# Optimization experiments

Hardware: AMD Instinct MI355X
Metric: run time of the kernel (lower is better)

The kernel has to match this reference:

```python
import jax, jax.numpy as jnp
import numpy as np

B, C, D, H, W = 1, 128, 8, 32, 32
NH, HD = 8, 16            # num_heads, head_dim = C // NH
PD, PH, PW = 2, 4, 4      # local patch dims
RD, RH, RW = 2, 2, 2      # global K/V reduction ratios
MLPH = 4 * C              # mlp_ratio = 4
EPS = 1e-5
SCALE = HD ** -0.5


def setup_inputs() -> dict:
    key = jax.random.key(0)
    ks = iter(jax.random.split(key, 16))
    def w(shape, scale=0.02):
        return jax.random.normal(next(ks), shape, jnp.float32) * scale
    inp = {"x": jax.random.normal(next(ks), (B, C, D, H, W), jnp.float32)}
    for p in ("l", "g"):  # local branch / global branch transformer blocks
        inp[f"{p}_n1_g"] = jnp.ones((C,), jnp.float32)
        inp[f"{p}_n1_b"] = jnp.zeros((C,), jnp.float32)
        inp[f"{p}_qkv_w"] = w((3 * C, C))            # Linear(dim, 3*dim, bias=False)
        inp[f"{p}_proj_w"] = w((C, C))
        inp[f"{p}_proj_b"] = jnp.zeros((C,), jnp.float32)
        inp[f"{p}_n2_g"] = jnp.ones((C,), jnp.float32)
        inp[f"{p}_n2_b"] = jnp.zeros((C,), jnp.float32)
        inp[f"{p}_fc1_w"] = w((MLPH, C))
        inp[f"{p}_fc1_b"] = jnp.zeros((MLPH,), jnp.float32)
        inp[f"{p}_fc2_w"] = w((C, MLPH))
        inp[f"{p}_fc2_b"] = jnp.zeros((C,), jnp.float32)
    inp["g_ke_w"] = w((C, C, RD, RH, RW))  # Conv3d(dim, dim, k=stride=(2,2,2), bias=False)
    inp["g_ve_w"] = w((C, C, RD, RH, RW))
    inp["g_nk_g"] = jnp.ones((HD,), jnp.float32)
    inp["g_nk_b"] = jnp.zeros((HD,), jnp.float32)
    inp["g_nv_g"] = jnp.ones((HD,), jnp.float32)
    inp["g_nv_b"] = jnp.zeros((HD,), jnp.float32)
    return inp


def _ln(t, g, b):
    m = t.mean(-1, keepdims=True)
    v = jnp.square(t - m).mean(-1, keepdims=True)
    return (t - m) * jax.lax.rsqrt(v + EPS) * g + b


def _mlp(t, w1, b1, w2, b2):
    return jax.nn.gelu(t @ w1.T + b1, approximate=False) @ w2.T + b2


def _forward(x, l_n1_g, l_n1_b, l_qkv_w, l_proj_w, l_proj_b, l_n2_g, l_n2_b,
             l_fc1_w, l_fc1_b, l_fc2_w, l_fc2_b,
             g_n1_g, g_n1_b, g_qkv_w, g_ke_w, g_ve_w, g_nk_g, g_nk_b,
             g_nv_g, g_nv_b, g_proj_w, g_proj_b, g_n2_g, g_n2_b,
             g_fc1_w, g_fc1_b, g_fc2_w, g_fc2_b):
    nd, nh, nw = D // PD, H // PH, W // PW
    R, Npl = nd * nh * nw, PD * PH * PW
    N = D * H * W

    # ---------------- Local branch ----------------
    # (B,C,D,H,W) -> (B, R, Npl, C) patch tokens
    loc = x.reshape(B, C, nd, PD, nh, PH, nw, PW)
    loc = loc.transpose(0, 2, 4, 6, 3, 5, 7, 1).reshape(B, R, Npl, C)
    y = _ln(loc, l_n1_g, l_n1_b)
    qkv = (y @ l_qkv_w.T).reshape(B, R, Npl, 3, NH, HD).transpose(3, 0, 1, 4, 2, 5)
    q, k, v = qkv[0], qkv[1], qkv[2]  # (B,R,NH,Npl,HD)
    attn = jax.nn.softmax(jnp.einsum('brhnd,brhmd->brhnm', q, k) * SCALE, axis=-1)
    o = jnp.einsum('brhnm,brhmd->brhnd', attn, v)
    # faithful to torch: (attn@v).transpose(-1,-2).reshape(B,R,Npl,C)
    o = jnp.swapaxes(o, -1, -2).reshape(B, R, Npl, C)
    loc = loc + (o @ l_proj_w.T + l_proj_b)
    loc = loc + _mlp(_ln(loc, l_n2_g, l_n2_b), l_fc1_w, l_fc1_b, l_fc2_w, l_fc2_b)
    # back to (B,C,D,H,W)
    loc_y = loc.reshape(B, nd, nh, nw, PD, PH, PW, C)
    loc_y = loc_y.transpose(0, 7, 1, 4, 2, 5, 3, 6).reshape(B, C, D, H, W)

    # ---------------- Global branch ----------------
    g = x.reshape(B, C, N).transpose(0, 2, 1)  # (B,N,C)
    y = _ln(g, g_n1_g, g_n1_b)
    qkv = y @ g_qkv_w.T  # (B,N,3C)
    q, k, v = jnp.split(qkv, 3, axis=-1)
    qh = q.reshape(B, N, NH, HD).transpose(0, 2, 1, 3)  # (B,NH,N,HD)
    dn = ('NCDHW', 'OIDHW', 'NCDHW')
    def _reduce(t, wc):
        tm = t.transpose(0, 2, 1).reshape(B, C, D, H, W)
        tr = jax.lax.conv_general_dilated(tm, wc, (RD, RH, RW), 'VALID',
                                          dimension_numbers=dn)
        nr = tr.shape[2] * tr.shape[3] * tr.shape[4]
        return tr.reshape(B, C, nr).transpose(0, 2, 1).reshape(B, nr, NH, HD).transpose(0, 2, 1, 3)
    kr = _ln(_reduce(k, g_ke_w), g_nk_g, g_nk_b)  # (B,NH,Nr,HD)
    vr = _ln(_reduce(v, g_ve_w), g_nv_g, g_nv_b)
    attn = jax.nn.softmax(jnp.einsum('bhnd,bhmd->bhnm', qh, kr) * SCALE, axis=-1)
    o = jnp.einsum('bhnm,bhmd->bhnd', attn, vr)
    o = o.transpose(0, 2, 1, 3).reshape(B, N, C)
    g = g + (o @ g_proj_w.T + g_proj_b)
    g = g + _mlp(_ln(g, g_n2_g, g_n2_b), g_fc1_w, g_fc1_b, g_fc2_w, g_fc2_b)
    glo_y = g.transpose(0, 2, 1).reshape(B, C, D, H, W)

    # ---------------- Gate ----------------
    return x * jax.nn.sigmoid(loc_y + glo_y)


def reference(x, l_n1_g, l_n1_b, l_qkv_w, l_proj_w, l_proj_b, l_n2_g, l_n2_b,
              l_fc1_w, l_fc1_b, l_fc2_w, l_fc2_b,
              g_n1_g, g_n1_b, g_qkv_w, g_ke_w, g_ve_w, g_nk_g, g_nk_b,
              g_nv_g, g_nv_b, g_proj_w, g_proj_b, g_n2_g, g_n2_b,
              g_fc1_w, g_fc1_b, g_fc2_w, g_fc2_b):
    return _forward(x, l_n1_g, l_n1_b, l_qkv_w, l_proj_w, l_proj_b, l_n2_g, l_n2_b,
                    l_fc1_w, l_fc1_b, l_fc2_w, l_fc2_b,
                    g_n1_g, g_n1_b, g_qkv_w, g_ke_w, g_ve_w, g_nk_g, g_nk_b,
                    g_nv_g, g_nv_b, g_proj_w, g_proj_b, g_n2_g, g_n2_b,
                    g_fc1_w, g_fc1_b, g_fc2_w, g_fc2_b)
```

## Files before the change

kernel.cpp:

```cpp
#include <hip/hip_runtime.h>
#include <math.h>

#define N_TOK 8192
#define C_DIM 128
#define NHD   8
#define HDIM  16
#define NR    1024
#define EPSV  1e-5f
#define QK_SCALE 0.25f

typedef __attribute__((ext_vector_type(8))) short short8;
typedef __attribute__((ext_vector_type(4))) float f32x4;

__device__ __forceinline__ float gelu_f(float v) {
    return 0.5f * v * (1.0f + erff(v * 0.70710678118654752f));
}
__device__ __forceinline__ float uaf(unsigned int u) {
    union { unsigned int u; float f; } x; x.u = u; return x.f;
}
__device__ __forceinline__ short f2b(float v) {
    union { float f; unsigned int u; } x; x.f = v;
    unsigned int r = x.u + 0x7fffu + ((x.u >> 16) & 1u);
    return (short)(r >> 16);
}
__device__ __forceinline__ void ld16bf(const short* p, float* d) {
    uint4 a = *(const uint4*)p;
    uint4 b = *(const uint4*)(p + 8);
    d[0]  = uaf(a.x << 16); d[1]  = uaf(a.x & 0xffff0000u);
    d[2]  = uaf(a.y << 16); d[3]  = uaf(a.y & 0xffff0000u);
    d[4]  = uaf(a.z << 16); d[5]  = uaf(a.z & 0xffff0000u);
    d[6]  = uaf(a.w << 16); d[7]  = uaf(a.w & 0xffff0000u);
    d[8]  = uaf(b.x << 16); d[9]  = uaf(b.x & 0xffff0000u);
    d[10] = uaf(b.y << 16); d[11] = uaf(b.y & 0xffff0000u);
    d[12] = uaf(b.z << 16); d[13] = uaf(b.z & 0xffff0000u);
    d[14] = uaf(b.w << 16); d[15] = uaf(b.w & 0xffff0000u);
}

struct CvtDesc { const float* src; short* dst; int n; int pad; };
struct CvtArgs { CvtDesc d[10]; };
__global__ __launch_bounds__(256) void cvtw_k(CvtArgs a) {
    CvtDesc dd = a.d[blockIdx.y];
    for (int i = blockIdx.x * 256 + threadIdx.x; i < dd.n; i += gridDim.x * 256)
        dd.dst[i] = f2b(dd.src[i]);
}

__global__ __launch_bounds__(256) void transpose_k(const float* __restrict__ x,
                                                   float* __restrict__ xt) {
    __shared__ float tile[32][33];
    int n0 = blockIdx.x * 32, c0 = blockIdx.y * 32;
    int tx = threadIdx.x, ty = threadIdx.y;
#pragma unroll
    for (int k = 0; k < 4; ++k)
        tile[ty + k * 8][tx] = x[(size_t)(c0 + ty + k * 8) * N_TOK + n0 + tx];
    __syncthreads();
#pragma unroll
    for (int k = 0; k < 4; ++k)
        xt[(size_t)(n0 + ty + k * 8) * C_DIM + c0 + tx] = tile[tx][ty + k * 8];
}

__global__ __launch_bounds__(256) void ln_token_k(const float* __restrict__ in,
                                                  const float* __restrict__ g1, const float* __restrict__ b1,
                                                  short* __restrict__ o1,
                                                  const float* __restrict__ g2, const float* __restrict__ b2,
                                                  short* __restrict__ o2) {
    int lane = threadIdx.x & 63;
    int n = blockIdx.x * 4 + (threadIdx.x >> 6);
    float v0 = in[(size_t)n * C_DIM + lane];
    float v1 = in[(size_t)n * C_DIM + 64 + lane];
    float s = v0 + v1, sq = v0 * v0 + v1 * v1;
#pragma unroll
    for (int off = 32; off >= 1; off >>= 1) {
        s += __shfl_xor(s, off);
        sq += __shfl_xor(sq, off);
    }
    float m = s * (1.0f / 128.0f);
    float var = sq * (1.0f / 128.0f) - m * m;
    float rs = rsqrtf(var + EPSV);
    float h0 = (v0 - m) * rs, h1 = (v1 - m) * rs;
    o1[(size_t)n * C_DIM + lane]      = f2b(h0 * g1[lane] + b1[lane]);
    o1[(size_t)n * C_DIM + 64 + lane] = f2b(h1 * g1[lane + 64] + b1[lane + 64]);
    o2[(size_t)n * C_DIM + lane]      = f2b(h0 * g2[lane] + b2[lane]);
    o2[(size_t)n * C_DIM + 64 + lane] = f2b(h1 * g2[lane + 64] + b2[lane + 64]);
}

__global__ __launch_bounds__(256) void ln2_pair_k(const float* __restrict__ in0,
                                                  const float* __restrict__ g0, const float* __restrict__ b0,
                                                  short* __restrict__ o0,
                                                  const float* __restrict__ in1,
                                                  const float* __restrict__ g1, const float* __restrict__ b1,
                                                  short* __restrict__ o1) {
    int blk = blockIdx.x;
    bool sel = blk >= 2048;
    blk &= 2047;
    const float* in = sel ? in1 : in0;
    const float* g  = sel ? g1 : g0;
    const float* b  = sel ? b1 : b0;
    short* o        = sel ? o1 : o0;
    int lane = threadIdx.x & 63;
    int n = blk * 4 + (threadIdx.x >> 6);
    float v0 = in[(size_t)n * C_DIM + lane];
    float v1 = in[(size_t)n * C_DIM + 64 + lane];
    float s = v0 + v1, sq = v0 * v0 + v1 * v1;
#pragma unroll
    for (int off = 32; off >= 1; off >>= 1) {
        s += __shfl_xor(s, off);
        sq += __shfl_xor(sq, off);
    }
    float m = s * (1.0f / 128.0f);
    float var = sq * (1.0f / 128.0f) - m * m;
    float rs = rsqrtf(var + EPSV);
    o[(size_t)n * C_DIM + lane]      = f2b((v0 - m) * rs * g[lane] + b[lane]);
    o[(size_t)n * C_DIM + 64 + lane] = f2b((v1 - m) * rs * g[lane + 64] + b[lane + 64]);
}

struct MArgs {
    const short* A[2]; const short* W[2];
    const float* bias[2]; const float* res[2];
    void* out[2];
};
template <int EPI>
__global__ __launch_bounds__(256) void mgemm_k(MArgs ga, int M, int N, int K, int kslice) {
    int zi    = (EPI == 3) ? (blockIdx.z >> 2) : blockIdx.z;
    int slice = (EPI == 3) ? (blockIdx.z & 3) : 0;
    const short* A = ga.A[zi];
    const short* W = ga.W[zi];
    __shared__ short As[128 * 64];
    __shared__ short Bs[128 * 64];
    int t = threadIdx.x;
    int w = t >> 6, l = t & 63;
    int m0 = blockIdx.x * 128, n0 = blockIdx.y * 128;
    int wm = (w >> 1) * 64, wn = (w & 1) * 64;
    int kbeg = (EPI == 3) ? slice * kslice : 0;
    int kend = kbeg + ((EPI == 3) ? kslice : K);

    f32x4 acc[4][4];
#pragma unroll
    for (int a = 0; a < 4; ++a)
#pragma unroll
        for (int b = 0; b < 4; ++b) acc[a][b] = f32x4{0.f, 0.f, 0.f, 0.f};

    for (int k0 = kbeg; k0 < kend; k0 += 64) {
        __syncthreads();
#pragma unroll
        for (int c = 0; c < 4; ++c) {
            int chunk = c * 256 + t;
            int row = chunk >> 3;
            int slot = chunk & 7;
            int ss = slot ^ (row & 7);
            uint4 av = *(const uint4*)(A + (size_t)(m0 + row) * K + k0 + slot * 8);
            *(uint4*)(As + row * 64 + ss * 8) = av;
            uint4 wv = *(const uint4*)(W + (size_t)(n0 + row) * K + k0 + slot * 8);
            *(uint4*)(Bs + row * 64 + ss * 8) = wv;
        }
        __syncthreads();
#pragma unroll
        for (int kk = 0; kk < 2; ++kk) {
            short8 af[4], bf[4];
            int sl = kk * 4 + (l >> 4);
#pragma unroll
            for (int mf = 0; mf < 4; ++mf) {
                int row = wm + mf * 16 + (l & 15);
                af[mf] = *(const short8*)(As + row * 64 + (sl ^ (row & 7)) * 8);
            }
#pragma unroll
            for (int nf = 0; nf < 4; ++nf) {
                int row = wn + nf * 16 + (l & 15);
                bf[nf] = *(const short8*)(Bs + row * 64 + (sl ^ (row & 7)) * 8);
            }
#pragma unroll
            for (int mf = 0; mf < 4; ++mf)
#pragma unroll
                for (int nf = 0; nf < 4; ++nf)
                    acc[mf][nf] = __builtin_amdgcn_mfma_f32_16x16x32_bf16(
                        af[mf], bf[nf], acc[mf][nf], 0, 0, 0);
        }
    }

#pragma unroll
    for (int mf = 0; mf < 4; ++mf) {
#pragma unroll
        for (int nf = 0; nf < 4; ++nf) {
            int col = n0 + wn + nf * 16 + (l & 15);
#pragma unroll
            for (int j = 0; j < 4; ++j) {
                int row = m0 + wm + mf * 16 + (l >> 4) * 4 + j;
                float v = acc[mf][nf][j];
                if (EPI == 0) {
                    ((short*)ga.out[zi])[(size_t)row * N + col] = f2b(v);
                } else if (EPI == 1) {
                    v += ga.bias[zi][col] + ga.res[zi][(size_t)row * N + col];
                    ((float*)ga.out[zi])[(size_t)row * N + col] = v;
                } else if (EPI == 2) {
                    v = gelu_f(v + ga.bias[zi][col]);
                    ((short*)ga.out[zi])[(size_t)row * N + col] = f2b(v);
                } else {
                    ((float*)ga.out[zi])[(size_t)slice * M * N + (size_t)row * N + col] = v;
                }
            }
        }
    }
}

__global__ __launch_bounds__(256) void local_attn_k(const short* __restrict__ qkv,
                                                    short* __restrict__ ob) {
    __shared__ float ks[NHD][32][HDIM];
    __shared__ float vs[NHD][32][HDIM];
    int m = threadIdx.x, h = threadIdx.y, r = blockIdx.x;
    int zd = r >> 6, zh = (r >> 3) & 7, zw = r & 7;
    int pd = m >> 4, ph = (m >> 2) & 3, pw = m & 3;
    int n = (zd * 2 + pd) * 1024 + (zh * 4 + ph) * 32 + (zw * 4 + pw);
    const short* base = qkv + (size_t)n * 384 + h * HDIM;
    float q[16], kt[16], vt[16];
    ld16bf(base, q);
    ld16bf(base + 128, kt);
    ld16bf(base + 256, vt);
#pragma unroll
    for (int d = 0; d < 16; ++d) { ks[h][m][d] = kt[d]; vs[h][m][d] = vt[d]; }
    __syncthreads();
    float s[32];
#pragma unroll
    for (int j = 0; j < 32; ++j) {
        float d = 0.f;
#pragma unroll
        for (int dd = 0; dd < 16; ++dd) d += q[dd] * ks[h][j][dd];
        s[j] = __expf(d * QK_SCALE);
    }
    float sum = 0.f;
#pragma unroll
    for (int j = 0; j < 32; ++j) sum += s[j];
    float inv = 1.0f / sum;
    float oo[16] = {};
#pragma unroll
    for (int j = 0; j < 32; ++j) {
        float p = s[j] * inv;
#pragma unroll
        for (int dd = 0; dd < 16; ++dd) oo[dd] += p * vs[h][j][dd];
    }
#pragma unroll
    for (int dd = 0; dd < 16; ++dd) {
        int n2 = h * 4 + (dd >> 2);
        int c2 = (dd & 3) * 32 + m;
        int pd2 = n2 >> 4, ph2 = (n2 >> 2) & 3, pw2 = n2 & 3;
        int nn = (zd * 2 + pd2) * 1024 + (zh * 4 + ph2) * 32 + (zw * 4 + pw2);
        ob[(size_t)nn * C_DIM + c2] = f2b(oo[dd]);
    }
}

__global__ __launch_bounds__(256) void gather_k(const short* __restrict__ qkv,
                                                short* __restrict__ kg, short* __restrict__ vg) {
    int idx = blockIdx.x * 256 + threadIdx.x;
    int nr = idx >> 10, qq = idx & 1023;
    int ci = qq >> 3, off = qq & 7;
    int od = off >> 2, oh = (off >> 1) & 1, ow = off & 1;
    int d2 = nr >> 8, h2 = (nr >> 4) & 15, w2 = nr & 15;
    int n = (2 * d2 + od) * 1024 + (2 * h2 + oh) * 32 + (2 * w2 + ow);
    kg[idx] = qkv[(size_t)n * 384 + 128 + ci];
    vg[idx] = qkv[(size_t)n * 384 + 256 + ci];
}

__global__ __launch_bounds__(256) void ln_head_sum_k(const float* __restrict__ kpart,
                                                     const float* __restrict__ vpart,
                                                     const float* __restrict__ gk, const float* __restrict__ bk,
                                                     const float* __restrict__ gv, const float* __restrict__ bv,
                                                     short* __restrict__ kout, short* __restrict__ vout) {
    int idx = blockIdx.x * 256 + threadIdx.x;
    bool sel = idx >= 8192;
    int id2 = idx & 8191;
    const float* part = sel ? vpart : kpart;
    const float* g    = sel ? gv : gk;
    const float* b    = sel ? bv : bk;
    int nr = id2 >> 3, h = id2 & 7;
    size_t base = (size_t)nr * C_DIM + h * HDIM;
    float v[16] = {};
#pragma unroll
    for (int p = 0; p < 4; ++p) {
        const float* pp = part + (size_t)p * (NR * C_DIM) + base;
#pragma unroll
        for (int d4 = 0; d4 < 4; ++d4) {
            float4 t = *(const float4*)(pp + d4 * 4);
            v[d4 * 4 + 0] += t.x; v[d4 * 4 + 1] += t.y;
            v[d4 * 4 + 2] += t.z; v[d4 * 4 + 3] += t.w;
        }
    }
    float s = 0.f;
#pragma unroll
    for (int i = 0; i < 16; ++i) s += v[i];
    float m = s * (1.0f / 16.0f);
    float sq = 0.f;
#pragma unroll
    for (int i = 0; i < 16; ++i) { float d = v[i] - m; sq += d * d; }
    float rs = rsqrtf(sq * (1.0f / 16.0f) + EPSV);
    if (!sel) {
        short* op = kout + (size_t)h * (NR * HDIM) + (size_t)nr * HDIM;
#pragma unroll
        for (int i = 0; i < 16; ++i)
            op[i] = f2b(((v[i] - m) * rs * g[i] + b[i]) * QK_SCALE);
    } else {
        short* op = vout + (size_t)h * (HDIM * NR) + nr;
#pragma unroll
        for (int i = 0; i < 16; ++i)
            op[(size_t)i * NR] = f2b((v[i] - m) * rs * g[i] + b[i]);
    }
}

__global__ __launch_bounds__(256) void gattn_k(const short* __restrict__ qkv,
                                               const short* __restrict__ kb,
                                               const short* __restrict__ vt,
                                               short* __restrict__ ob) {
    __shared__ short plds[4][2048];
    int t = threadIdx.x;
    int w = t >> 6, l = t & 63;
    int h = blockIdx.y;
    int lr = l & 15, lq = l >> 4;
    int q0 = blockIdx.x * 64 + w * 16;

    short8 qf = short8{0, 0, 0, 0, 0, 0, 0, 0};
    if (lq < 2)
        qf = *(const short8*)(qkv + (size_t)(q0 + lr) * 384 + h * HDIM + lq * 8);

    const short* kh = kb + (size_t)h * (NR * HDIM);
    const short* vh = vt + (size_t)h * (HDIM * NR);
    short* pw = &plds[w][0];

    const f32x4 zz = {0.f, 0.f, 0.f, 0.f};
    f32x4 oacc = {0.f, 0.f, 0.f, 0.f};
    float rs0 = 0.f, rs1 = 0.f, rs2 = 0.f, rs3 = 0.f;

    for (int c = 0; c < 8; ++c) {
        int kbase = c * 128;
        f32x4 s[8];
#pragma unroll
        for (int nf = 0; nf < 8; ++nf) {
            short8 kf = short8{0, 0, 0, 0, 0, 0, 0, 0};
            if (lq < 2)
                kf = *(const short8*)(kh + (size_t)(kbase + nf * 16 + lr) * HDIM + lq * 8);
            s[nf] = __builtin_amdgcn_mfma_f32_16x16x32_bf16(qf, kf, zz, 0, 0, 0);
        }
#pragma unroll
        for (int nf = 0; nf < 8; ++nf) {
            int key = nf * 16 + lr;
            float p0 = __expf(s[nf][0]);
            float p1 = __expf(s[nf][1]);
            float p2 = __expf(s[nf][2]);
            float p3 = __expf(s[nf][3]);
            rs0 += p0; rs1 += p1; rs2 += p2; rs3 += p3;
            int q_ = lq * 4;
            pw[((q_ + 0) * 128 + key) ^ (((q_ + 0) & 7) << 3)] = f2b(p0);
            pw[((q_ + 1) * 128 + key) ^ (((q_ + 1) & 7) << 3)] = f2b(p1);
            pw[((q_ + 2) * 128 + key) ^ (((q_ + 2) & 7) << 3)] = f2b(p2);
            pw[((q_ + 3) * 128 + key) ^ (((q_ + 3) & 7) << 3)] = f2b(p3);
        }
#pragma unroll
        for (int ks = 0; ks < 4; ++ks) {
            short8 pf = *(const short8*)&pw[(lr * 128 + ks * 32 + lq * 8) ^ ((lr & 7) << 3)];
            short8 vf = *(const short8*)(vh + (size_t)lr * NR + kbase + ks * 32 + lq * 8);
            oacc = __builtin_amdgcn_mfma_f32_16x16x32_bf16(pf, vf, oacc, 0, 0, 0);
        }
    }
#pragma unroll
    for (int off = 1; off <= 8; off <<= 1) {
        rs0 += __shfl_xor(rs0, off);
        rs1 += __shfl_xor(rs1, off);
        rs2 += __shfl_xor(rs2, off);
        rs3 += __shfl_xor(rs3, off);
    }
    size_t base_o = (size_t)(q0 + lq * 4) * C_DIM + h * HDIM + lr;
    ob[base_o]             = f2b(oacc[0] / rs0);
    ob[base_o + C_DIM]     = f2b(oacc[1] / rs1);
    ob[base_o + 2 * C_DIM] = f2b(oacc[2] / rs2);
    ob[base_o + 3 * C_DIM] = f2b(oacc[3] / rs3);
}

__global__ __launch_bounds__(256) void gate_k(const float* __restrict__ x,
                                              const float* __restrict__ lf, const float* __restrict__ gf,
                                              float* __restrict__ out) {
    __shared__ float tile[32][33];
    int n0 = blockIdx.x * 32, c0 = blockIdx.y * 32;
    int tx = threadIdx.x, ty = threadIdx.y;
#pragma unroll
    for (int k = 0; k < 4; ++k) {
        int n = n0 + ty + k * 8, c = c0 + tx;
        tile[ty + k * 8][tx] = lf[(size_t)n * C_DIM + c] + gf[(size_t)n * C_DIM + c];
    }
    __syncthreads();
#pragma unroll
    for (int k = 0; k < 4; ++k) {
        int c = c0 + ty + k * 8, n = n0 + tx;
        float z = tile[tx][ty + k * 8];
        float sg = 1.0f / (1.0f + __expf(-z));
        out[(size_t)c * N_TOK + n] = x[(size_t)c * N_TOK + n] * sg;
    }
}

extern "C" void kernel_launch(void* const* d_in, const int* in_sizes, int n_in,
                              void* d_out, int out_size, void* d_ws, size_t ws_size,
                              hipStream_t stream) {
    const float* x        = (const float*)d_in[0];
    const float* l_n1_g   = (const float*)d_in[1];
    const float* l_n1_b   = (const float*)d_in[2];
    const float* l_qkv_w  = (const float*)d_in[3];
    const float* l_proj_w = (const float*)d_in[4];
    const float* l_proj_b = (const float*)d_in[5];
    const float* l_n2_g   = (const float*)d_in[6];
    const float* l_n2_b   = (const float*)d_in[7];
    const float* l_fc1_w  = (const float*)d_in[8];
    const float* l_fc1_b  = (const float*)d_in[9];
    const float* l_fc2_w  = (const float*)d_in[10];
    const float* l_fc2_b  = (const float*)d_in[11];
    const float* g_n1_g   = (const float*)d_in[12];
    const float* g_n1_b   = (const float*)d_in[13];
    const float* g_qkv_w  = (const float*)d_in[14];
    const float* g_proj_w = (const float*)d_in[15];
    const float* g_proj_b = (const float*)d_in[16];
    const float* g_n2_g   = (const float*)d_in[17];
    const float* g_n2_b   = (const float*)d_in[18];
    const float* g_fc1_w  = (const float*)d_in[19];
    const float* g_fc1_b  = (const float*)d_in[20];
    const float* g_fc2_w  = (const float*)d_in[21];
    const float* g_fc2_b  = (const float*)d_in[22];
    const float* g_ke_w   = (const float*)d_in[23];
    const float* g_ve_w   = (const float*)d_in[24];
    const float* g_nk_g   = (const float*)d_in[25];
    const float* g_nk_b   = (const float*)d_in[26];
    const float* g_nv_g   = (const float*)d_in[27];
    const float* g_nv_b   = (const float*)d_in[28];
    float* out = (float*)d_out;

    char* base = (char*)d_ws;
    float* xt     = (float*)(base);
    float* t1_l   = (float*)(base + (4ull  << 20));
    float* t1_g   = (float*)(base + (8ull  << 20));
    short* yA16   = (short*)(base + (12ull << 20));
    short* yG16   = (short*)(base + (14ull << 20));
    short* t2_l   = yA16;
    short* t2_g   = yG16;
    float* locfin = (float*)(base + (12ull << 20));
    short* obuf_l = (short*)(base + (16ull << 20));
    short* obuf_g = (short*)(base + (18ull << 20));
    float* glofin = (float*)(base + (16ull << 20));
    short* qkv_l  = (short*)(base + (20ull << 20));
    short* qkv_g  = (short*)(base + (26ull << 20));
    short* h1_l   = (short*)(base + (32ull << 20));
    float* kpart  = (float*)(base + (32ull << 20));
    float* vpart  = (float*)(base + (34ull << 20));
    short* h1_g   = (short*)(base + (40ull << 20));
    short* kg16   = (short*)(base + (40ull << 20));
    short* vg16   = (short*)(base + (42ull << 20));
    short* kb16   = (short*)(base + (48ull << 20));
    short* vt16   = (short*)(base + (48ull << 20) + (512ull << 10));
    short* wts    = (short*)(base + (49ull << 20));

    const int L_QKV = 0,      L_PROJ = 49152, L_FC1 = 65536,  L_FC2 = 131072;
    const int G_QKV = 196608, G_PROJ = 245760, G_FC1 = 262144, G_FC2 = 327680;
    const int G_KE  = 393216, G_VE   = 524288;

    CvtArgs ca;
    ca.d[0] = {l_qkv_w,  wts + L_QKV,  49152, 0};
    ca.d[1] = {l_proj_w, wts + L_PROJ, 16384, 0};
    ca.d[2] = {l_fc1_w,  wts + L_FC1,  65536, 0};
    ca.d[3] = {l_fc2_w,  wts + L_FC2,  65536, 0};
    ca.d[4] = {g_qkv_w,  wts + G_QKV,  49152, 0};
    ca.d[5] = {g_proj_w, wts + G_PROJ, 16384, 0};
    ca.d[6] = {g_fc1_w,  wts + G_FC1,  65536, 0};
    ca.d[7] = {g_fc2_w,  wts + G_FC2,  65536, 0};
    ca.d[8] = {g_ke_w,   wts + G_KE,  131072, 0};
    ca.d[9] = {g_ve_w,   wts + G_VE,  131072, 0};

    cvtw_k<<<dim3(32, 10), 256, 0, stream>>>(ca);
    transpose_k<<<dim3(256, 4), dim3(32, 8), 0, stream>>>(x, xt);
    ln_token_k<<<2048, 256, 0, stream>>>(xt, l_n1_g, l_n1_b, yA16, g_n1_g, g_n1_b, yG16);

    MArgs a_qkv = {{yA16, yG16}, {wts + L_QKV, wts + G_QKV}, {nullptr, nullptr}, {nullptr, nullptr}, {qkv_l, qkv_g}};
    mgemm_k<0><<<dim3(64, 3, 2), 256, 0, stream>>>(a_qkv, N_TOK, 384, 128, 0);

    local_attn_k<<<256, dim3(32, 8), 0, stream>>>(qkv_l, obuf_l);
    gather_k<<<4096, 256, 0, stream>>>(qkv_g, kg16, vg16);

    MArgs a_cv = {{kg16, vg16}, {wts + G_KE, wts + G_VE}, {nullptr, nullptr}, {nullptr, nullptr}, {kpart, vpart}};
    mgemm_k<3><<<dim3(8, 1, 8), 256, 0, stream>>>(a_cv, NR, 128, 1024, 256);

    ln_head_sum_k<<<64, 256, 0, stream>>>(kpart, vpart, g_nk_g, g_nk_b, g_nv_g, g_nv_b, kb16, vt16);

    gattn_k<<<dim3(128, 8), 256, 0, stream>>>(qkv_g, kb16, vt16, obuf_g);

    MArgs a_pj = {{obuf_l, obuf_g}, {wts + L_PROJ, wts + G_PROJ}, {l_proj_b, g_proj_b}, {xt, xt}, {t1_l, t1_g}};
    mgemm_k<1><<<dim3(64, 1, 2), 256, 0, stream>>>(a_pj, N_TOK, 128, 128, 0);

    ln2_pair_k<<<4096, 256, 0, stream>>>(t1_l, l_n2_g, l_n2_b, t2_l, t1_g, g_n2_g, g_n2_b, t2_g);

    MArgs a_f1 = {{t2_l, t2_g}, {wts + L_FC1, wts + G_FC1}, {l_fc1_b, g_fc1_b}, {nullptr, nullptr}, {h1_l, h1_g}};
    mgemm_k<2><<<dim3(64, 4, 2), 256, 0, stream>>>(a_f1, N_TOK, 512, 128, 0);

    MArgs a_f2 = {{h1_l, h1_g}, {wts + L_FC2, wts + G_FC2}, {l_fc2_b, g_fc2_b}, {t1_l, t1_g}, {locfin, glofin}};
    mgemm_k<1><<<dim3(64, 1, 2), 256, 0, stream>>>(a_f2, N_TOK, 128, 512, 0);

    gate_k<<<dim3(256, 4), dim3(32, 8), 0, stream>>>(x, locfin, glofin, out);
}
```

Measured before the change: 143.8 us.

## Increase split-K for reduction conv GEMM and streamline global attention softmax

```diff
diff --git a/kernel.cpp b/kernel.cpp
--- a/kernel.cpp
+++ b/kernel.cpp
@@ -8,6 +8,7 @@
 #define NR    1024
 #define EPSV  1e-5f
 #define QK_SCALE 0.25f
+#define QK_L2E  0.36067376f
 
 typedef __attribute__((ext_vector_type(8))) short short8;
 typedef __attribute__((ext_vector_type(4))) float f32x4;
@@ -120,8 +121,8 @@
 };
 template <int EPI>
 __global__ __launch_bounds__(256) void mgemm_k(MArgs ga, int M, int N, int K, int kslice) {
-    int zi    = (EPI == 3) ? (blockIdx.z >> 2) : blockIdx.z;
-    int slice = (EPI == 3) ? (blockIdx.z & 3) : 0;
+    int zi    = (EPI == 3) ? (blockIdx.z >> 3) : blockIdx.z;
+    int slice = (EPI == 3) ? (blockIdx.z & 7) : 0;
     const short* A = ga.A[zi];
     const short* W = ga.W[zi];
     __shared__ short As[128 * 64];
@@ -273,7 +274,7 @@
     size_t base = (size_t)nr * C_DIM + h * HDIM;
     float v[16] = {};
 #pragma unroll
-    for (int p = 0; p < 4; ++p) {
+    for (int p = 0; p < 8; ++p) {
         const float* pp = part + (size_t)p * (NR * C_DIM) + base;
 #pragma unroll
         for (int d4 = 0; d4 < 4; ++d4) {
@@ -294,7 +295,7 @@
         short* op = kout + (size_t)h * (NR * HDIM) + (size_t)nr * HDIM;
 #pragma unroll
         for (int i = 0; i < 16; ++i)
-            op[i] = f2b(((v[i] - m) * rs * g[i] + b[i]) * QK_SCALE);
+            op[i] = f2b(((v[i] - m) * rs * g[i] + b[i]) * QK_L2E);
     } else {
         short* op = vout + (size_t)h * (HDIM * NR) + nr;
 #pragma unroll
@@ -324,7 +325,7 @@
 
     const f32x4 zz = {0.f, 0.f, 0.f, 0.f};
     f32x4 oacc = {0.f, 0.f, 0.f, 0.f};
-    float rs0 = 0.f, rs1 = 0.f, rs2 = 0.f, rs3 = 0.f;
+    float rs = 0.f;
 
     for (int c = 0; c < 8; ++c) {
         int kbase = c * 128;
@@ -334,21 +335,22 @@
             short8 kf = short8{0, 0, 0, 0, 0, 0, 0, 0};
             if (lq < 2)
                 kf = *(const short8*)(kh + (size_t)(kbase + nf * 16 + lr) * HDIM + lq * 8);
-            s[nf] = __builtin_amdgcn_mfma_f32_16x16x32_bf16(qf, kf, zz, 0, 0, 0);
+            s[nf] = __builtin_amdgcn_mfma_f32_16x16x32_bf16(kf, qf, zz, 0, 0, 0);
         }
 #pragma unroll
         for (int nf = 0; nf < 8; ++nf) {
-            int key = nf * 16 + lr;
-            float p0 = __expf(s[nf][0]);
-            float p1 = __expf(s[nf][1]);
-            float p2 = __expf(s[nf][2]);
-            float p3 = __expf(s[nf][3]);
-            rs0 += p0; rs1 += p1; rs2 += p2; rs3 += p3;
-            int q_ = lq * 4;
-            pw[((q_ + 0) * 128 + key) ^ (((q_ + 0) & 7) << 3)] = f2b(p0);
-            pw[((q_ + 1) * 128 + key) ^ (((q_ + 1) & 7) << 3)] = f2b(p1);
-            pw[((q_ + 2) * 128 + key) ^ (((q_ + 2) & 7) << 3)] = f2b(p2);
-            pw[((q_ + 3) * 128 + key) ^ (((q_ + 3) & 7) << 3)] = f2b(p3);
+            float p0 = exp2f(s[nf][0]);
+            float p1 = exp2f(s[nf][1]);
+            float p2 = exp2f(s[nf][2]);
+            float p3 = exp2f(s[nf][3]);
+            rs += (p0 + p1) + (p2 + p3);
+            unsigned int u01, u23;
+            asm("v_cvt_pk_bf16_f32 %0, %1, %2" : "=v"(u01) : "v"(p0), "v"(p1));
+            asm("v_cvt_pk_bf16_f32 %0, %1, %2" : "=v"(u23) : "v"(p2), "v"(p3));
+            int k0 = nf * 16 + lq * 4;
+            int sw = (lr & 7) << 3;
+            *(unsigned int*)&pw[lr * 128 + (k0 ^ sw)]       = u01;
+            *(unsigned int*)&pw[lr * 128 + ((k0 + 2) ^ sw)] = u23;
         }
 #pragma unroll
         for (int ks = 0; ks < 4; ++ks) {
@@ -357,18 +359,17 @@
             oacc = __builtin_amdgcn_mfma_f32_16x16x32_bf16(pf, vf, oacc, 0, 0, 0);
         }
     }
-#pragma unroll
-    for (int off = 1; off <= 8; off <<= 1) {
-        rs0 += __shfl_xor(rs0, off);
-        rs1 += __shfl_xor(rs1, off);
-        rs2 += __shfl_xor(rs2, off);
-        rs3 += __shfl_xor(rs3, off);
-    }
+    rs += __shfl_xor(rs, 16);
+    rs += __shfl_xor(rs, 32);
+    float r0 = __shfl(rs, lq * 4 + 0);
+    float r1 = __shfl(rs, lq * 4 + 1);
+    float r2 = __shfl(rs, lq * 4 + 2);
+    float r3 = __shfl(rs, lq * 4 + 3);
     size_t base_o = (size_t)(q0 + lq * 4) * C_DIM + h * HDIM + lr;
-    ob[base_o]             = f2b(oacc[0] / rs0);
-    ob[base_o + C_DIM]     = f2b(oacc[1] / rs1);
-    ob[base_o + 2 * C_DIM] = f2b(oacc[2] / rs2);
-    ob[base_o + 3 * C_DIM] = f2b(oacc[3] / rs3);
+    ob[base_o]             = f2b(oacc[0] / r0);
+    ob[base_o + C_DIM]     = f2b(oacc[1] / r1);
+    ob[base_o + 2 * C_DIM] = f2b(oacc[2] / r2);
+    ob[base_o + 3 * C_DIM] = f2b(oacc[3] / r3);
 }
 
 __global__ __launch_bounds__(256) void gate_k(const float* __restrict__ x,
@@ -442,7 +443,7 @@
     short* qkv_g  = (short*)(base + (26ull << 20));
     short* h1_l   = (short*)(base + (32ull << 20));
     float* kpart  = (float*)(base + (32ull << 20));
-    float* vpart  = (float*)(base + (34ull << 20));
+    float* vpart  = (float*)(base + (36ull << 20));
     short* h1_g   = (short*)(base + (40ull << 20));
     short* kg16   = (short*)(base + (40ull << 20));
     short* vg16   = (short*)(base + (42ull << 20));
@@ -477,7 +478,7 @@
     gather_k<<<4096, 256, 0, stream>>>(qkv_g, kg16, vg16);
 
     MArgs a_cv = {{kg16, vg16}, {wts + G_KE, wts + G_VE}, {nullptr, nullptr}, {nullptr, nullptr}, {kpart, vpart}};
-    mgemm_k<3><<<dim3(8, 1, 8), 256, 0, stream>>>(a_cv, NR, 128, 1024, 256);
+    mgemm_k<3><<<dim3(8, 1, 16), 256, 0, stream>>>(a_cv, NR, 128, 1024, 128);
 
     ln_head_sum_k<<<64, 256, 0, stream>>>(kpart, vpart, g_nk_g, g_nk_b, g_nv_g, g_nv_b, kb16, vt16);
 
```

Result: no change. 144.0 us (+0.1%).
